# Kernel tuning notes

Measured on AMD Instinct MI355X. Metric: run time of the kernel, lower is better.

The kernel has to match this reference:

```python
import jax, jax.numpy as jnp
import numpy as np

BETA = 0.1  # 0.1 + 0.1*sin(t/1000) at t=0

def setup_inputs() -> dict:
    key = jax.random.key(0)
    k1, k2 = jax.random.split(key)
    x_cat = jax.random.uniform(k1, (256, 64, 64), dtype=jnp.float32, minval=1e-6, maxval=1.0)
    u = jax.random.uniform(k2, (256, 64, 64), dtype=jnp.float32, minval=1e-6, maxval=1.0 - 1e-6)
    noise = -jnp.log(-jnp.log(u))  # standard Gumbel(0,1)
    return {"x_cat": x_cat, "noise": noise}

def reference(x_cat, noise):
    B, A, k = x_cat.shape
    P = A // 2
    x = x_cat.reshape(B, P, 2, k)          # [B,P,2,k]: axis 0 = horiz, 1 = vert
    h, v = x[:, :, 0], x[:, :, 1]
    # outer product per (batch, place): [B,P,k] x [B,P,k] -> [B,P,k,k]
    places = jnp.einsum('bpj,bpk->bpjk', h, v)
    # Gumbel-argmax sampling: pdf * 1[log(pdf)+beta*g == max over k]
    log_pdf = jnp.log(x) + BETA * noise.reshape(B, P, 2, k)
    mx = jnp.max(log_pdf, axis=-1, keepdims=True)
    sampled = x * (log_pdf == mx).astype(x.dtype)
    sampled_points = jnp.einsum('bpj,bpk->bpjk', sampled[:, :, 0], sampled[:, :, 1]) * 100.0
    return (places, sampled_points)
```

## Files before the change

kernel.cpp:

```cpp
#include <hip/hip_runtime.h>
#include <math.h>


#define BETA 0.1f
#define PLACES_ELEMS 33554432ull

__global__ __launch_bounds__(256) void spatial_sampler_kernel(
    const float* __restrict__ x_cat,
    const float* __restrict__ noise,
    float* __restrict__ out)
{
    const int bp   = blockIdx.x;
    const int t    = threadIdx.x;
    const int wave = t >> 6;
    const int lane = t & 63;

    const float* xrow = x_cat + (size_t)bp * 128;
    const float* nrow = noise + (size_t)bp * 128;

    __shared__ float sh[64];
    __shared__ float sv[64];
    __shared__ int   s_max[2];

    if (wave < 2) {
        const int base = wave * 64;
        float x = xrow[base + lane];
        if (wave == 0) sh[lane] = x; else sv[lane] = x;

        float lp  = logf(x) + BETA * nrow[base + lane];
        int   idx = lane;
        #pragma unroll
        for (int off = 32; off > 0; off >>= 1) {
            float o_lp  = __shfl_xor(lp, off, 64);
            int   o_idx = __shfl_xor(idx, off, 64);
            if (o_lp > lp || (o_lp == lp && o_idx < idx)) { lp = o_lp; idx = o_idx; }
        }
        if (lane == 0) s_max[wave] = idx;
    }
    __syncthreads();

    const int jmax = s_max[0];
    const int kmax = s_max[1];

    float4* __restrict__ places  = (float4*)out + (size_t)bp * 1024;
    float4* __restrict__ sampled = (float4*)(out + PLACES_ELEMS) + (size_t)bp * 1024;

    #pragma unroll
    for (int i = 0; i < 4; ++i) {
        const int f = i * 256 + t;
        const int j = f >> 4;
        const int c = (f & 15) << 2;

        const float hj = sh[j];
        float4 p;
        p.x = hj * sv[c + 0];
        p.y = hj * sv[c + 1];
        p.z = hj * sv[c + 2];
        p.w = hj * sv[c + 3];
        places[f] = p;

        float4 sp = make_float4(0.f, 0.f, 0.f, 0.f);
        if (j == jmax) {
            if (c + 0 == kmax) sp.x = p.x * 100.f;
            if (c + 1 == kmax) sp.y = p.y * 100.f;
            if (c + 2 == kmax) sp.z = p.z * 100.f;
            if (c + 3 == kmax) sp.w = p.w * 100.f;
        }
        sampled[f] = sp;
    }
}

extern "C" void kernel_launch(void* const* d_in, const int* in_sizes, int n_in,
                              void* d_out, int out_size, void* d_ws, size_t ws_size,
                              hipStream_t stream) {
    const float* x_cat = (const float*)d_in[0];
    const float* noise = (const float*)d_in[1];
    float* out = (float*)d_out;

    spatial_sampler_kernel<<<dim3(8192), dim3(256), 0, stream>>>(x_cat, noise, out);
}
```

Baseline: 265.6 us.

## Zero sampled output via memset and write only argmax element plus nontemporal stores

```diff
diff --git a/kernel.cpp b/kernel.cpp
--- a/kernel.cpp
+++ b/kernel.cpp
@@ -5,7 +5,9 @@
 #define BETA 0.1f
 #define PLACES_ELEMS 33554432ull
 
-__global__ __launch_bounds__(256) void spatial_sampler_kernel(
+typedef float vfloat4 __attribute__((ext_vector_type(4)));
+
+__global__ __launch_bounds__(256) void places_argmax_kernel(
     const float* __restrict__ x_cat,
     const float* __restrict__ noise,
     float* __restrict__ out)
@@ -23,11 +25,11 @@
     __shared__ int   s_max[2];
 
     if (wave < 2) {
-        const int base = wave * 64;
-        float x = xrow[base + lane];
+        const int base = wave * 64 + lane;
+        float x = xrow[base];
         if (wave == 0) sh[lane] = x; else sv[lane] = x;
 
-        float lp  = logf(x) + BETA * nrow[base + lane];
+        float lp  = logf(x) + BETA * nrow[base];
         int   idx = lane;
         #pragma unroll
         for (int off = 32; off > 0; off >>= 1) {
@@ -39,34 +41,24 @@
     }
     __syncthreads();
 
-    const int jmax = s_max[0];
-    const int kmax = s_max[1];
+    const int     c     = t & 15;
+    const int     jbase = t >> 4;
+    const vfloat4 v4    = ((const vfloat4*)sv)[c];
 
-    float4* __restrict__ places  = (float4*)out + (size_t)bp * 1024;
-    float4* __restrict__ sampled = (float4*)(out + PLACES_ELEMS) + (size_t)bp * 1024;
+    vfloat4* __restrict__ places = (vfloat4*)out + (size_t)bp * 1024;
 
     #pragma unroll
     for (int i = 0; i < 4; ++i) {
-        const int f = i * 256 + t;
-        const int j = f >> 4;
-        const int c = (f & 15) << 2;
+        const float hj = sh[i * 16 + jbase];
+        vfloat4 p = hj * v4;
+        __builtin_nontemporal_store(p, &places[i * 256 + t]);
+    }
 
-        const float hj = sh[j];
-        float4 p;
-        p.x = hj * sv[c + 0];
-        p.y = hj * sv[c + 1];
-        p.z = hj * sv[c + 2];
-        p.w = hj * sv[c + 3];
-        places[f] = p;
-
-        float4 sp = make_float4(0.f, 0.f, 0.f, 0.f);
-        if (j == jmax) {
-            if (c + 0 == kmax) sp.x = p.x * 100.f;
-            if (c + 1 == kmax) sp.y = p.y * 100.f;
-            if (c + 2 == kmax) sp.z = p.z * 100.f;
-            if (c + 3 == kmax) sp.w = p.w * 100.f;
-        }
-        sampled[f] = sp;
+    if (t == 0) {
+        const int jmax = s_max[0];
+        const int kmax = s_max[1];
+        out[PLACES_ELEMS + (size_t)bp * 4096 + (size_t)(jmax * 64 + kmax)] =
+            100.0f * sh[jmax] * sv[kmax];
     }
 }
 
@@ -77,5 +69,8 @@
     const float* noise = (const float*)d_in[1];
     float* out = (float*)d_out;
 
-    spatial_sampler_kernel<<<dim3(8192), dim3(256), 0, stream>>>(x_cat, noise, out);
+    (void)hipMemsetAsync((void*)(out + PLACES_ELEMS), 0,
+                         PLACES_ELEMS * sizeof(float), stream);
+
+    places_argmax_kernel<<<dim3(8192), dim3(256), 0, stream>>>(x_cat, noise, out);
 }
```

Result: no change. 266.3 us (+0.3%).
